# Optimization experiments

Hardware: AMD Instinct MI355X
Metric: run time of the kernel (lower is better)

## Reference

```python
import jax, jax.numpy as jnp
import numpy as np

HEADS = 16
D_MODEL = 1024
D_K = D_MODEL // HEADS


def setup_inputs() -> dict:
    key = jax.random.key(0)
    ks = jax.random.split(key, 12)
    B, S = 4, 2048
    scale = 1.0 / np.sqrt(D_MODEL)
    inp = {
        'q': jax.random.normal(ks[0], (B, S, D_MODEL), jnp.float32),
        'k': jax.random.normal(ks[1], (B, S, D_MODEL), jnp.float32),
        'v': jax.random.normal(ks[2], (B, S, D_MODEL), jnp.float32),
        'Wq': jax.random.normal(ks[3], (D_MODEL, D_MODEL), jnp.float32) * scale,
        'bq': jnp.zeros((D_MODEL,), jnp.float32),
        'Wk': jax.random.normal(ks[4], (D_MODEL, D_MODEL), jnp.float32) * scale,
        'bk': jnp.zeros((D_MODEL,), jnp.float32),
        'Wv': jax.random.normal(ks[5], (D_MODEL, D_MODEL), jnp.float32) * scale,
        'bv': jnp.zeros((D_MODEL,), jnp.float32),
        'Wo': jax.random.normal(ks[6], (D_MODEL, D_MODEL), jnp.float32) * scale,
        'bo': jnp.zeros((D_MODEL,), jnp.float32),
    }
    return inp


def reference(q, k, v, Wq, bq, Wk, bk, Wv, bv, Wo, bo):
    B, S, _ = q.shape
    # linear projections, split into heads: [B, H, S, Dk]
    def proj(x, W, b):
        return (x @ W.T + b).reshape(B, -1, HEADS, D_K).transpose(0, 2, 1, 3)
    qh = proj(q, Wq, bq)
    kh = proj(k, Wk, bk)
    vh = proj(v, Wv, bv)
    scores = jnp.einsum('bhsd,bhtd->bhst', qh, kh) / jnp.sqrt(jnp.float32(D_K))
    attn = jax.nn.softmax(scores, axis=-1)
    ctx = jnp.einsum('bhst,bhtd->bhsd', attn, vh)  # [B,H,S,Dk]
    concat = ctx.transpose(0, 2, 1, 3).reshape(B, S, D_MODEL)
    return concat @ Wo.T + bo
```

## Files before the change

### kernel.cpp

```cpp
#include <hip/hip_runtime.h>
#include <hip/hip_bf16.h>


typedef __attribute__((ext_vector_type(8))) short short8;
typedef __attribute__((ext_vector_type(4))) float f32x4;
typedef __attribute__((ext_vector_type(16))) float f32x16;

#define DEV __device__ __forceinline__

DEV ushort f2bf(float f) {
  union { float f; unsigned u; } v; v.f = f;
  return (ushort)((v.u + 0x7fffu + ((v.u >> 16) & 1u)) >> 16);
}

DEV void gload_lds16(const void* g, void* lds) {
  __builtin_amdgcn_global_load_lds(
      (const __attribute__((address_space(1))) void*)g,
      (__attribute__((address_space(3))) void*)lds, 16, 0, 0);
}

DEV short8 pk8(float4 v0, float4 v1) {
  unsigned u0, u1, u2, u3;
  asm("v_cvt_pk_bf16_f32 %0, %1, %2" : "=v"(u0) : "v"(v0.x), "v"(v0.y));
  asm("v_cvt_pk_bf16_f32 %0, %1, %2" : "=v"(u1) : "v"(v0.z), "v"(v0.w));
  asm("v_cvt_pk_bf16_f32 %0, %1, %2" : "=v"(u2) : "v"(v1.x), "v"(v1.y));
  asm("v_cvt_pk_bf16_f32 %0, %1, %2" : "=v"(u3) : "v"(v1.z), "v"(v1.w));
  union { unsigned u[4]; short8 s; } r;
  r.u[0] = u0; r.u[1] = u1; r.u[2] = u2; r.u[3] = u3;
  return r.s;
}

__global__ void cvtx_kernel(const float* __restrict__ a, const float* __restrict__ b,
                            const float* __restrict__ c,
                            ushort* __restrict__ oa, ushort* __restrict__ ob,
                            ushort* __restrict__ oc, int n8) {
  const float* s[3] = {a, b, c};
  ushort* o[3] = {oa, ob, oc};
  const float* src = s[blockIdx.y];
  ushort* dst = o[blockIdx.y];
  int stride = gridDim.x * blockDim.x;
  for (int i = blockIdx.x * blockDim.x + threadIdx.x; i < n8; i += stride) {
    float4 v0 = ((const float4*)src)[2 * i];
    float4 v1 = ((const float4*)src)[2 * i + 1];
    ((short8*)dst)[i] = pk8(v0, v1);
  }
}

__global__ void cvtw_kernel(const float* __restrict__ a, const float* __restrict__ b,
                            const float* __restrict__ c, const float* __restrict__ d,
                            ushort* __restrict__ oa, ushort* __restrict__ ob,
                            ushort* __restrict__ oc, ushort* __restrict__ od, int n8) {
  const float* s[4] = {a, b, c, d};
  ushort* o[4] = {oa, ob, oc, od};
  const float* src = s[blockIdx.y];
  ushort* dst = o[blockIdx.y];
  int stride = gridDim.x * blockDim.x;
  for (int i = blockIdx.x * blockDim.x + threadIdx.x; i < n8; i += stride) {
    float4 v0 = ((const float4*)src)[2 * i];
    float4 v1 = ((const float4*)src)[2 * i + 1];
    ((short8*)dst)[i] = pk8(v0, v1);
  }
}

template<int MODE>
__global__ __launch_bounds__(512, 4) void gemm_bt(
    const ushort* __restrict__ X, const ushort* __restrict__ W,
    const float* __restrict__ bias, void* __restrict__ out)
{
  constexpr int K = 1024, N = 1024;
  __shared__ __align__(16) ushort As[128 * 64];
  __shared__ __align__(16) ushort Bs[128 * 64];
  const int t = threadIdx.x;
  const int w = t >> 6, l = t & 63;
  const int bid = blockIdx.x;
  const int m0 = (bid >> 3) * 128, n0 = (bid & 7) * 128;
  const int wm = (w & 1) * 64, wn = (w >> 1) * 32;

  const f32x4 zero = {0.f, 0.f, 0.f, 0.f};
  f32x4 acc[4][2];
#pragma unroll
  for (int i = 0; i < 4; i++)
#pragma unroll
    for (int j = 0; j < 2; j++) acc[i][j] = zero;

  const int srow = t >> 3;
  const int scol = ((t & 7) ^ (srow & 7)) << 4;
  const char* xg = (const char*)X + (size_t)(m0 + srow) * 2048 + scol;
  const char* wg = (const char*)W + (size_t)(n0 + srow) * 2048 + scol;
  char* asl = (char*)As + t * 16;
  char* bsl = (char*)Bs + t * 16;

  const int swf = (l & 7) << 4;

  for (int kt = 0; kt < K; kt += 64) {
    __syncthreads();
#pragma unroll
    for (int pass = 0; pass < 2; pass++) {
      gload_lds16(xg + (size_t)pass * 64 * 2048 + kt * 2, asl + pass * 8192);
      gload_lds16(wg + (size_t)pass * 64 * 2048 + kt * 2, bsl + pass * 8192);
    }
    __syncthreads();

#pragma unroll
    for (int h = 0; h < 2; h++) {
      short8 af[4], bf[2];
#pragma unroll
      for (int i = 0; i < 4; i++) {
        int ra = wm + i * 16 + (l & 15);
        int cb = (h * 64 + (l >> 4) * 16) ^ swf;
        af[i] = *(const short8*)((const char*)As + ra * 128 + cb);
      }
#pragma unroll
      for (int j = 0; j < 2; j++) {
        int rb = wn + j * 16 + (l & 15);
        int cb = (h * 64 + (l >> 4) * 16) ^ swf;
        bf[j] = *(const short8*)((const char*)Bs + rb * 128 + cb);
      }
#pragma unroll
      for (int i = 0; i < 4; i++)
#pragma unroll
        for (int j = 0; j < 2; j++)
          acc[i][j] = __builtin_amdgcn_mfma_f32_16x16x32_bf16(af[i], bf[j], acc[i][j], 0, 0, 0);
    }
  }

#pragma unroll
  for (int i = 0; i < 4; i++) {
    int mbase = m0 + wm + i * 16 + ((l >> 4) << 2);
#pragma unroll
    for (int j = 0; j < 2; j++) {
      int n = n0 + wn + j * 16 + (l & 15);
      float bv = bias[n];
#pragma unroll
      for (int r = 0; r < 4; r++) {
        int m = mbase + r;
        float v = acc[i][j][r] + bv;
        if (MODE == 2) {
          ((float*)out)[(size_t)m * N + n] = v;
        } else {
          int b = m >> 11, s = m & 2047;
          int h = n >> 6, d = n & 63;
          size_t off;
          if (MODE == 0) off = ((size_t)(b * 16 + h) * 2048 + s) * 64 + d;
          else           off = ((size_t)(b * 16 + h) * 64 + d) * 2048 + s;
          ((ushort*)out)[off] = f2bf(v);
        }
      }
    }
  }
}

__global__ __launch_bounds__(512, 4) void attn_kernel(
    const ushort* __restrict__ Qh, const ushort* __restrict__ Kh,
    const ushort* __restrict__ Vt, ushort* __restrict__ ctx)
{
  __shared__ __align__(16) ushort Ks[2 * 2 * 64 * 64];
  __shared__ __align__(16) ushort Vs[2 * 2 * 64 * 64];
  const int t = threadIdx.x, w = t >> 6, l = t & 63;
  const int hf = l >> 5, ln = l & 31;
  const int p = blockIdx.x;
  const int logical = (p & 7) * 64 + (p >> 3);
  const int bh = logical >> 3;
  const int q0 = (logical & 7) * 256 + w * 32;
  const ushort* Qb = Qh + (size_t)bh * 2048 * 64;
  const ushort* Kb = Kh + (size_t)bh * 2048 * 64;
  const ushort* Vb = Vt + (size_t)bh * 64 * 2048;

  short8 qb[4];
  {
    const ushort* qp = Qb + (size_t)(q0 + ln) * 64 + hf * 8;
    const float SC = 0.18033688f;
#pragma unroll
    for (int s = 0; s < 4; s++) {
      short8 v = *(const short8*)(qp + s * 16);
#pragma unroll
      for (int j = 0; j < 8; j++) {
        union { float f; unsigned u; } x;
        x.u = ((unsigned)(ushort)v[j]) << 16;
        x.f *= SC;
        v[j] = (short)f2bf(x.f);
      }
      qb[s] = v;
    }
  }

  short8 ones;
#pragma unroll
  for (int j = 0; j < 8; j++) ones[j] = (short)0x3F80;

  f32x16 o_acc[2], o_l;
  f32x16 z16;
#pragma unroll
  for (int r = 0; r < 16; r++) z16[r] = 0.f;
  o_acc[0] = z16; o_acc[1] = z16; o_l = z16;

  const int srow = t >> 3;
  const int ssw = (((t & 7) ^ (srow & 7)) << 4);
  const char* kg = (const char*)Kb + (size_t)srow * 128 + ssw;
  const char* vg = (const char*)Vb + (size_t)srow * 4096 + ssw;
  char* kld = (char*)Ks + (size_t)t * 16;
  char* vld = (char*)Vs + (size_t)t * 16;

#define STAGE(buf_, kv0_) do {                                              \
    gload_lds16(kg + (size_t)(kv0_) * 128, kld + (buf_) * 16384);           \
    gload_lds16(kg + (size_t)(kv0_) * 128 + 8192, kld + (buf_) * 16384 + 8192); \
    gload_lds16(vg + (size_t)(kv0_) * 2, vld + (buf_) * 16384);             \
    gload_lds16(vg + (size_t)(kv0_) * 2 + 128, vld + (buf_) * 16384 + 8192);\
  } while (0)

  STAGE(0, 0);
  __syncthreads();

  const int rsw = (ln & 7) << 4;

  for (int it = 0; it < 16; it++) {
    const int cur = it & 1;
    if (it < 15) STAGE(cur ^ 1, (it + 1) * 128);

#pragma unroll
    for (int sub = 0; sub < 2; sub++) {
      const char* KsB = (const char*)Ks + cur * 16384 + sub * 8192;
      const char* VsB = (const char*)Vs + cur * 16384 + sub * 8192;

      f32x16 sf[2];
      __builtin_amdgcn_s_setprio(1);
#pragma unroll
      for (int f = 0; f < 2; f++) {
        f32x16 s_ = z16;
#pragma unroll
        for (int s = 0; s < 4; s++) {
          short8 kf = *(const short8*)(KsB + (32 * f + ln) * 128 + ((16 * hf + 32 * s) ^ rsw));
          s_ = __builtin_amdgcn_mfma_f32_32x32x16_bf16(kf, qb[s], s_, 0, 0, 0);
        }
        sf[f] = s_;
      }
      __builtin_amdgcn_s_setprio(0);

#pragma unroll
      for (int f = 0; f < 2; f++)
#pragma unroll
        for (int r = 0; r < 16; r++) sf[f][r] = __builtin_amdgcn_exp2f(sf[f][r]);

      __builtin_amdgcn_s_setprio(1);
#pragma unroll
      for (int f = 0; f < 2; f++) {
        unsigned wd0, wd1, wd2, wd3, wd4, wd5, wd6, wd7;
        asm("v_cvt_pk_bf16_f32 %0, %1, %2" : "=v"(wd0) : "v"(sf[f][0]),  "v"(sf[f][1]));
        asm("v_cvt_pk_bf16_f32 %0, %1, %2" : "=v"(wd1) : "v"(sf[f][2]),  "v"(sf[f][3]));
        asm("v_cvt_pk_bf16_f32 %0, %1, %2" : "=v"(wd2) : "v"(sf[f][4]),  "v"(sf[f][5]));
        asm("v_cvt_pk_bf16_f32 %0, %1, %2" : "=v"(wd3) : "v"(sf[f][6]),  "v"(sf[f][7]));
        asm("v_cvt_pk_bf16_f32 %0, %1, %2" : "=v"(wd4) : "v"(sf[f][8]),  "v"(sf[f][9]));
        asm("v_cvt_pk_bf16_f32 %0, %1, %2" : "=v"(wd5) : "v"(sf[f][10]), "v"(sf[f][11]));
        asm("v_cvt_pk_bf16_f32 %0, %1, %2" : "=v"(wd6) : "v"(sf[f][12]), "v"(sf[f][13]));
        asm("v_cvt_pk_bf16_f32 %0, %1, %2" : "=v"(wd7) : "v"(sf[f][14]), "v"(sf[f][15]));
        asm("v_permlane32_swap_b32 %0, %1" : "+v"(wd0), "+v"(wd2));
        asm("v_permlane32_swap_b32 %0, %1" : "+v"(wd1), "+v"(wd3));
        asm("v_permlane32_swap_b32 %0, %1" : "+v"(wd4), "+v"(wd6));
        asm("v_permlane32_swap_b32 %0, %1" : "+v"(wd5), "+v"(wd7));
#pragma unroll
        for (int s2 = 0; s2 < 2; s2++) {
          union { unsigned u[4]; short8 s8; } pa;
          if (s2 == 0) { pa.u[0] = wd0; pa.u[1] = wd1; pa.u[2] = wd2; pa.u[3] = wd3; }
          else         { pa.u[0] = wd4; pa.u[1] = wd5; pa.u[2] = wd6; pa.u[3] = wd7; }
          const int s = 2 * f + s2;
#pragma unroll
          for (int dn = 0; dn < 2; dn++) {
            short8 vf = *(const short8*)(VsB + (32 * dn + ln) * 128 + ((16 * hf + 32 * s) ^ rsw));
            o_acc[dn] = __builtin_amdgcn_mfma_f32_32x32x16_bf16(pa.s8, vf, o_acc[dn], 0, 0, 0);
          }
          o_l = __builtin_amdgcn_mfma_f32_32x32x16_bf16(pa.s8, ones, o_l, 0, 0, 0);
        }
      }
      __builtin_amdgcn_s_setprio(0);
    }

    __syncthreads();
  }
#undef STAGE

  const int b = bh >> 4, hd = bh & 15;
#pragma unroll
  for (int r = 0; r < 16; r++) {
    int qrow = (r & 3) + 8 * (r >> 2) + 4 * hf;
    float inv = 1.f / o_l[r];
#pragma unroll
    for (int dn = 0; dn < 2; dn++) {
      int d = dn * 32 + ln;
      size_t off = (((size_t)b * 2048 + (q0 + qrow)) * 16 + hd) * 64 + d;
      ctx[off] = f2bf(o_acc[dn][r] * inv);
    }
  }
}

extern "C" void kernel_launch(void* const* d_in, const int* in_sizes, int n_in,
                              void* d_out, int out_size, void* d_ws, size_t ws_size,
                              hipStream_t stream) {
  const float* q  = (const float*)d_in[0];
  const float* k  = (const float*)d_in[1];
  const float* v  = (const float*)d_in[2];
  const float* Wq = (const float*)d_in[3];
  const float* bq = (const float*)d_in[4];
  const float* Wk = (const float*)d_in[5];
  const float* bk = (const float*)d_in[6];
  const float* Wv = (const float*)d_in[7];
  const float* bv = (const float*)d_in[8];
  const float* Wo = (const float*)d_in[9];
  const float* bo = (const float*)d_in[10];

  const size_t MSZ = (size_t)8192 * 1024;
  const size_t WSZ = (size_t)1024 * 1024;
  char* ws = (char*)d_ws;

  if (ws_size >= (size_t)106 * 1024 * 1024) {
    ushort* qb16 = (ushort*)ws;
    ushort* kb16 = qb16 + MSZ;
    ushort* vb16 = kb16 + MSZ;
    ushort* w16_0 = vb16 + MSZ;
    ushort* w16_1 = w16_0 + WSZ;
    ushort* w16_2 = w16_1 + WSZ;
    ushort* w16_3 = w16_2 + WSZ;
    ushort* Qhb = w16_3 + WSZ;
    ushort* Khb = Qhb + MSZ;
    ushort* Vtb = Khb + MSZ;
    ushort* ctx = qb16;

    cvtw_kernel<<<dim3(128, 4), 256, 0, stream>>>(Wq, Wk, Wv, Wo,
                                                  w16_0, w16_1, w16_2, w16_3,
                                                  (int)(WSZ / 8));
    cvtx_kernel<<<dim3(1024, 3), 256, 0, stream>>>(q, k, v, qb16, kb16, vb16,
                                                   (int)(MSZ / 8));
    gemm_bt<0><<<512, 512, 0, stream>>>(qb16, w16_0, bq, Qhb);
    gemm_bt<0><<<512, 512, 0, stream>>>(kb16, w16_1, bk, Khb);
    gemm_bt<1><<<512, 512, 0, stream>>>(vb16, w16_2, bv, Vtb);
    attn_kernel<<<dim3(512), 512, 0, stream>>>(Qhb, Khb, Vtb, ctx);
    gemm_bt<2><<<512, 512, 0, stream>>>(ctx, w16_3, bo, (float*)d_out);
  } else {
    ushort* Xbuf = (ushort*)ws;
    ushort* w16_0 = Xbuf + MSZ;
    ushort* w16_1 = w16_0 + WSZ;
    ushort* w16_2 = w16_1 + WSZ;
    ushort* w16_3 = w16_2 + WSZ;
    ushort* Qhb = w16_3 + WSZ;
    ushort* Khb = Qhb + MSZ;
    ushort* Vtb = Khb + MSZ;
    ushort* ctx = Xbuf;

    cvtw_kernel<<<dim3(128, 4), 256, 0, stream>>>(Wq, Wk, Wv, Wo,
                                                  w16_0, w16_1, w16_2, w16_3,
                                                  (int)(WSZ / 8));
    cvtx_kernel<<<dim3(1024, 1), 256, 0, stream>>>(q, q, q, Xbuf, Xbuf, Xbuf,
                                                   (int)(MSZ / 8));
    gemm_bt<0><<<512, 512, 0, stream>>>(Xbuf, w16_0, bq, Qhb);
    cvtx_kernel<<<dim3(1024, 1), 256, 0, stream>>>(k, k, k, Xbuf, Xbuf, Xbuf,
                                                   (int)(MSZ / 8));
    gemm_bt<0><<<512, 512, 0, stream>>>(Xbuf, w16_1, bk, Khb);
    cvtx_kernel<<<dim3(1024, 1), 256, 0, stream>>>(v, v, v, Xbuf, Xbuf, Xbuf,
                                                   (int)(MSZ / 8));
    gemm_bt<1><<<512, 512, 0, stream>>>(Xbuf, w16_2, bv, Vtb);
    attn_kernel<<<dim3(512), 512, 0, stream>>>(Qhb, Khb, Vtb, ctx);
    gemm_bt<2><<<512, 512, 0, stream>>>(ctx, w16_3, bo, (float*)d_out);
  }
}
```

Baseline: 205.4 us.

## Double-buffer LDS tiles in projection GEMM to overlap loads with MFMA

```diff
diff --git a/kernel.cpp b/kernel.cpp
--- a/kernel.cpp
+++ b/kernel.cpp
@@ -68,8 +68,8 @@
     const float* __restrict__ bias, void* __restrict__ out)
 {
   constexpr int K = 1024, N = 1024;
-  __shared__ __align__(16) ushort As[128 * 64];
-  __shared__ __align__(16) ushort Bs[128 * 64];
+  __shared__ __align__(16) ushort As[2 * 128 * 64];
+  __shared__ __align__(16) ushort Bs[2 * 128 * 64];
   const int t = threadIdx.x;
   const int w = t >> 6, l = t & 63;
   const int bid = blockIdx.x;
@@ -90,16 +90,26 @@
   char* asl = (char*)As + t * 16;
   char* bsl = (char*)Bs + t * 16;
 
+#define GSTAGE(buf_, kt_) do {                                                   \
+    _Pragma("unroll")                                                            \
+    for (int pass = 0; pass < 2; pass++) {                                       \
+      gload_lds16(xg + (size_t)pass * 64 * 2048 + (kt_) * 2,                     \
+                  asl + (buf_) * 16384 + pass * 8192);                           \
+      gload_lds16(wg + (size_t)pass * 64 * 2048 + (kt_) * 2,                     \
+                  bsl + (buf_) * 16384 + pass * 8192);                           \
+    }                                                                            \
+  } while (0)
+
   const int swf = (l & 7) << 4;
 
-  for (int kt = 0; kt < K; kt += 64) {
-    __syncthreads();
-#pragma unroll
-    for (int pass = 0; pass < 2; pass++) {
-      gload_lds16(xg + (size_t)pass * 64 * 2048 + kt * 2, asl + pass * 8192);
-      gload_lds16(wg + (size_t)pass * 64 * 2048 + kt * 2, bsl + pass * 8192);
-    }
-    __syncthreads();
+  GSTAGE(0, 0);
+  __syncthreads();
+
+  for (int step = 0; step < 16; step++) {
+    const int cur = step & 1;
+    if (step < 15) GSTAGE(cur ^ 1, (step + 1) * 64);
+    const char* AsB = (const char*)As + cur * 16384;
+    const char* BsB = (const char*)Bs + cur * 16384;
 
 #pragma unroll
     for (int h = 0; h < 2; h++) {
@@ -108,13 +118,13 @@
       for (int i = 0; i < 4; i++) {
         int ra = wm + i * 16 + (l & 15);
         int cb = (h * 64 + (l >> 4) * 16) ^ swf;
-        af[i] = *(const short8*)((const char*)As + ra * 128 + cb);
+        af[i] = *(const short8*)(AsB + ra * 128 + cb);
       }
 #pragma unroll
       for (int j = 0; j < 2; j++) {
         int rb = wn + j * 16 + (l & 15);
         int cb = (h * 64 + (l >> 4) * 16) ^ swf;
-        bf[j] = *(const short8*)((const char*)Bs + rb * 128 + cb);
+        bf[j] = *(const short8*)(BsB + rb * 128 + cb);
       }
 #pragma unroll
       for (int i = 0; i < 4; i++)
@@ -122,7 +132,10 @@
         for (int j = 0; j < 2; j++)
           acc[i][j] = __builtin_amdgcn_mfma_f32_16x16x32_bf16(af[i], bf[j], acc[i][j], 0, 0, 0);
     }
-  }
+
+    __syncthreads();
+  }
+#undef GSTAGE
 
 #pragma unroll
   for (int i = 0; i < 4; i++) {
```

Result: no change. 202.9 us (-1.2%).
